# Performance work log

Measured on AMD Instinct MI355X. Metric: run time of the kernel, lower is better.

## Reference

```python
import jax, jax.numpy as jnp
import numpy as np

BRANCH = 16   # children per internal node
DEPTH = 4     # levels 0..4, leaves at level 4
IN = 512
HID = 512

def _level_sizes():
    return [BRANCH ** d for d in range(DEPTH + 1)]

def setup_inputs() -> dict:
    key = jax.random.key(0)
    ks = jax.random.split(key, 9)
    N = sum(_level_sizes())  # 69905
    x = jax.random.normal(ks[0], (N, IN), dtype=jnp.float32)
    s = 1.0 / np.sqrt(IN + HID)  # torch nn.Linear default init bound
    def lin(kw, kb):
        w = jax.random.uniform(kw, (HID, IN + HID), jnp.float32, -s, s)
        b = jax.random.uniform(kb, (HID,), jnp.float32, -s, s)
        return w, b
    wi_w, wi_b = lin(ks[1], ks[2])
    wf_w, wf_b = lin(ks[3], ks[4])
    wo_w, wo_b = lin(ks[5], ks[6])
    wu_w, wu_b = lin(ks[7], ks[8])
    return {"x": x, "wi_w": wi_w, "wi_b": wi_b, "wf_w": wf_w, "wf_b": wf_b,
            "wo_w": wo_w, "wo_b": wo_b, "wu_w": wu_w, "wu_b": wu_b}

def reference(x, wi_w, wi_b, wf_w, wf_b, wo_w, wo_b, wu_w, wu_b):
    sizes = _level_sizes()
    offs = np.concatenate([[0], np.cumsum(sizes)])
    levels = [x[offs[d]:offs[d + 1]] for d in range(DEPTH + 1)]

    def gates(xh):
        i = jax.nn.sigmoid(xh @ wi_w.T + wi_b)
        o = jax.nn.sigmoid(xh @ wo_w.T + wo_b)
        u = jnp.tanh(xh @ wu_w.T + wu_b)
        return i, o, u

    # leaf_forward: h_prev = 0, no forget terms
    Xl = levels[DEPTH]
    xh = jnp.concatenate([Xl, jnp.zeros((Xl.shape[0], HID), Xl.dtype)], axis=1)
    i, o, u = gates(xh)
    C = i * u
    H = o * jnp.tanh(C)

    # node_forward, bottom-up. Faithful quirk of the source: the forget gate
    # is computed on the child CELL state (cat(x, c_k)), not the hidden state.
    for d in range(DEPTH - 1, -1, -1):
        Xd = levels[d]                      # [n, IN]
        n = Xd.shape[0]
        Hc = H.reshape(n, BRANCH, HID)      # children hidden
        Cc = C.reshape(n, BRANCH, HID)      # children cell
        h_sum = Hc.sum(axis=1)
        xh = jnp.concatenate([Xd, h_sum], axis=1)
        i, o, u = gates(xh)
        xc = jnp.concatenate([jnp.broadcast_to(Xd[:, None, :], (n, BRANCH, IN)), Cc], axis=-1)
        f = jax.nn.sigmoid(jnp.einsum('nbk,hk->nbh', xc, wf_w) + wf_b)
        C = i * u + (f * Cc).sum(axis=1)
        H = o * jnp.tanh(C)

    return H[0], C[0]
```

## Files before the change

kernel.cpp:

```cpp
#include <hip/hip_runtime.h>
#include <stdint.h>
#include <stddef.h>


typedef __bf16 bf16x8 __attribute__((ext_vector_type(8)));
typedef float  f32x4  __attribute__((ext_vector_type(4)));
typedef void __attribute__((address_space(3))) lds_void_t;
typedef void __attribute__((address_space(1))) gbl_void_t;

__device__ __forceinline__ uint16_t f2bf(float f) {
  union { __bf16 b; uint16_t u; } v;
  v.b = (__bf16)f;
  return v.u;
}
__device__ __forceinline__ float bf2f(uint16_t u) {
  union { uint32_t u; float f; } v; v.u = (uint32_t)u << 16;
  return v.f;
}
__device__ __forceinline__ float sig_(float x) {
  return __builtin_amdgcn_rcpf(1.0f + __expf(-x));
}
__device__ __forceinline__ float tanh_(float x) {
  return __builtin_fmaf(2.f,
      __builtin_amdgcn_rcpf(1.f + __expf(-2.f * x)), -1.f);
}

__global__ void k_conv_x(const float4* __restrict__ src,
                         ushort4* __restrict__ dst, long n4) {
  long i = blockIdx.x * (long)blockDim.x + threadIdx.x;
  long stride = (long)gridDim.x * blockDim.x;
  for (; i < n4; i += stride) {
    float4 v = src[i];
    ushort4 r;
    r.x = f2bf(v.x); r.y = f2bf(v.y); r.z = f2bf(v.z); r.w = f2bf(v.w);
    dst[i] = r;
  }
}
__global__ void k_conv_w(const float4* __restrict__ w0,
                         const float4* __restrict__ w1,
                         const float4* __restrict__ w2,
                         const float4* __restrict__ w3,
                         ushort4* __restrict__ dst) {
  const long per4 = (long)512 * 1024 / 4;
  long i = blockIdx.x * (long)blockDim.x + threadIdx.x;
  long stride = (long)gridDim.x * blockDim.x;
  for (; i < 4 * per4; i += stride) {
    long seg = i / per4, off2 = i - seg * per4;
    const float4* s = (seg == 0) ? w0 : (seg == 1) ? w1 : (seg == 2) ? w2 : w3;
    float4 v = s[off2];
    ushort4 r;
    r.x = f2bf(v.x); r.y = f2bf(v.y); r.z = f2bf(v.z); r.w = f2bf(v.w);
    dst[i] = r;
  }
}

#define BM 128
#define BN 128
#define BK 32

__global__ __launch_bounds__(256)
void k_gemm_bt(const uint16_t* __restrict__ A, int lda,
               const uint16_t* __restrict__ B, int ldb,
               float* __restrict__ C, int ldc, int K) {
  __shared__ uint16_t As[BM * BK];
  __shared__ uint16_t Bs[BN * BK];
  const int tid = threadIdx.x, lane = tid & 63, wave = tid >> 6;
  const int lrow = lane & 15, quad = lane >> 4;
  const int wm = (wave >> 1) * 64, wn = (wave & 1) * 64;
  const long tm = blockIdx.x, tn = blockIdx.y;
  f32x4 acc[4][4] = {};
  const int srow = lane >> 2, scol = (lane & 3) * 8;
  for (int k0 = 0; k0 < K; k0 += BK) {
#pragma unroll
    for (int i = 0; i < 2; ++i) {
      int row = i * 64 + wave * 16 + srow;
      const uint16_t* gp = A + (tm * BM + row) * (long)lda + k0 + scol;
      __builtin_amdgcn_global_load_lds((gbl_void_t*)(uintptr_t)gp,
          (lds_void_t*)&As[i * 2048 + wave * 512], 16, 0, 0);
    }
#pragma unroll
    for (int i = 0; i < 2; ++i) {
      int row = i * 64 + wave * 16 + srow;
      const uint16_t* gp = B + (tn * BN + row) * (long)ldb + k0 + scol;
      __builtin_amdgcn_global_load_lds((gbl_void_t*)(uintptr_t)gp,
          (lds_void_t*)&Bs[i * 2048 + wave * 512], 16, 0, 0);
    }
    __syncthreads();
    bf16x8 a[4], b[4];
#pragma unroll
    for (int f = 0; f < 4; ++f)
      a[f] = *(const bf16x8*)&As[(wm + f * 16 + lrow) * BK + quad * 8];
#pragma unroll
    for (int f = 0; f < 4; ++f)
      b[f] = *(const bf16x8*)&Bs[(wn + f * 16 + lrow) * BK + quad * 8];
#pragma unroll
    for (int fm = 0; fm < 4; ++fm)
#pragma unroll
      for (int fn = 0; fn < 4; ++fn)
        acc[fm][fn] = __builtin_amdgcn_mfma_f32_16x16x32_bf16(
            a[fm], b[fn], acc[fm][fn], 0, 0, 0);
    __syncthreads();
  }
#pragma unroll
  for (int fm = 0; fm < 4; ++fm)
#pragma unroll
    for (int fn = 0; fn < 4; ++fn) {
      long col  = tn * BN + wn + fn * 16 + lrow;
      long row0 = tm * BM + wm + fm * 16 + quad * 4;
#pragma unroll
      for (int r = 0; r < 4; ++r)
        C[(row0 + r) * (long)ldc + col] = acc[fm][fn][r];
    }
}

template <bool HAS_F>
__global__ __launch_bounds__(256, 3)
void k_level(const uint16_t* __restrict__ A, int lda, int K,
             const uint16_t* __restrict__ Wg,
             const float* __restrict__ bi, const float* __restrict__ bo,
             const float* __restrict__ bu,
             const float* __restrict__ Fpart,
             uint16_t* __restrict__ Cbf,
             const uint16_t* __restrict__ Xnext,
             uint16_t* __restrict__ xh_next) {
  __shared__ uint16_t As[128 * 64];
  __shared__ uint16_t Bs[192 * 64];
  const int tid = threadIdx.x, lane = tid & 63, wave = tid >> 6;
  const int lrow = lane & 15, quad = lane >> 4;
  const int wm = (wave >> 1) * 64, wn = (wave & 1) * 32;

  long tm, tn;
  {
    const int nTm = (int)(gridDim.x >> 3);
    int b = blockIdx.x;
    if ((nTm & 7) == 0) {
      int x = b & 7, j = b >> 3, per = nTm >> 3;
      tn = j & 7; tm = (long)x * per + (j >> 3);
    } else { tm = b >> 3; tn = b & 7; }
  }

  f32x4 acc[3][4][2] = {};

  const int srow = lane >> 3;
  const int scol = (((lane & 7) ^ srow) << 3);
  const int rsw = lrow & 7;
  const int pc[2] = { ((0 + quad) ^ rsw) << 3, ((4 + quad) ^ rsw) << 3 };

  for (int k0 = 0; k0 < K; k0 += 64) {
#pragma unroll
    for (int j = 0; j < 4; ++j) {
      int row = wave * 32 + j * 8 + srow;
      const uint16_t* gp = A + (tm * 128 + row) * (long)lda + k0 + scol;
      __builtin_amdgcn_global_load_lds((gbl_void_t*)(uintptr_t)gp,
          (lds_void_t*)&As[(wave * 32 + j * 8) * 64], 16, 0, 0);
    }
#pragma unroll
    for (int j = 0; j < 6; ++j) {
      int cc = wave * 6 + j;
      int g  = cc >> 3;
      long grow = (long)g * 512 + tn * 64 + (cc & 7) * 8 + srow;
      const uint16_t* gp = Wg + grow * 1024 + k0 + scol;
      __builtin_amdgcn_global_load_lds((gbl_void_t*)(uintptr_t)gp,
          (lds_void_t*)&Bs[cc * 512], 16, 0, 0);
    }
    __syncthreads();

#pragma unroll
    for (int h = 0; h < 2; ++h) {
      bf16x8 a[4];
#pragma unroll
      for (int f = 0; f < 4; ++f)
        a[f] = *(const bf16x8*)&As[(wm + f * 16 + lrow) * 64 + pc[h]];
#pragma unroll
      for (int g = 0; g < 3; ++g) {
        bf16x8 b0 = *(const bf16x8*)&Bs[(g * 64 + wn + lrow) * 64 + pc[h]];
        bf16x8 b1 = *(const bf16x8*)&Bs[(g * 64 + wn + 16 + lrow) * 64 +
                                        pc[h]];
#pragma unroll
        for (int fm = 0; fm < 4; ++fm) {
          acc[g][fm][0] = __builtin_amdgcn_mfma_f32_16x16x32_bf16(
              a[fm], b0, acc[g][fm][0], 0, 0, 0);
          acc[g][fm][1] = __builtin_amdgcn_mfma_f32_16x16x32_bf16(
              a[fm], b1, acc[g][fm][1], 0, 0, 0);
        }
      }
    }
    __syncthreads();
  }

#pragma unroll
  for (int fn = 0; fn < 2; ++fn) {
    long col = tn * 64 + wn + fn * 16 + lrow;
    float biv = bi[col], bov = bo[col], buv = bu[col];
#pragma unroll
    for (int fm = 0; fm < 4; ++fm) {
      long row0 = tm * 128 + wm + fm * 16 + quad * 4;
      long pg   = tm * 8 + (wm >> 4) + fm;
      float hs = 0.f;
#pragma unroll
      for (int r = 0; r < 4; ++r) {
        long row = row0 + r;
        float iv = sig_(acc[0][fm][fn][r] + biv);
        float ov = sig_(acc[1][fm][fn][r] + bov);
        float uv = tanh_(acc[2][fm][fn][r] + buv);
        float c  = iv * uv;
        if (HAS_F) c += Fpart[row * 512 + col];
        Cbf[row * 512 + col] = f2bf(c);
        hs += ov * tanh_(c);
      }
      hs += __shfl_xor(hs, 16, 64);
      hs += __shfl_xor(hs, 32, 64);
      if (quad == 0) {
        xh_next[pg * 1024 + col]       = Xnext[pg * 512 + col];
        xh_next[pg * 1024 + 512 + col] = f2bf(hs);
      }
    }
  }
}

__global__ __launch_bounds__(256, 3)
void k_fc_combine(const uint16_t* __restrict__ Cbf,
                  const uint16_t* __restrict__ Wfc, int ldb,
                  const float* __restrict__ Fx,
                  const float* __restrict__ bfb,
                  float* __restrict__ Fpart) {
  __shared__ uint16_t As[128 * 64];
  __shared__ uint16_t Bs[128 * 64];
  const int tid = threadIdx.x, lane = tid & 63, wave = tid >> 6;
  const int lrow = lane & 15, quad = lane >> 4;
  const int wm = (wave >> 1) * 64, wn = (wave & 1) * 64;
  long tm, tn;
  {
    const int nTm = (int)(gridDim.x >> 2);
    int b = blockIdx.x;
    if ((nTm & 7) == 0) {
      int x = b & 7, j = b >> 3, per = nTm >> 3;
      tn = j & 3; tm = (long)x * per + (j >> 2);
    } else { tm = b >> 2; tn = b & 3; }
  }
  const int lda = 512;
  f32x4 acc[4][4] = {};

  const int srow = lane >> 3;
  const int scol = (((lane & 7) ^ srow) << 3);
  const int rsw = lrow & 7;
  const int pc[2] = { ((0 + quad) ^ rsw) << 3, ((4 + quad) ^ rsw) << 3 };

  for (int k0 = 0; k0 < 512; k0 += 64) {
#pragma unroll
    for (int j = 0; j < 4; ++j) {
      int row = wave * 32 + j * 8 + srow;
      const uint16_t* gp = Cbf + (tm * BM + row) * (long)lda + k0 + scol;
      __builtin_amdgcn_global_load_lds((gbl_void_t*)(uintptr_t)gp,
          (lds_void_t*)&As[(wave * 32 + j * 8) * 64], 16, 0, 0);
    }
#pragma unroll
    for (int j = 0; j < 4; ++j) {
      int row = wave * 32 + j * 8 + srow;
      const uint16_t* gp = Wfc + (tn * BN + row) * (long)ldb + k0 + scol;
      __builtin_amdgcn_global_load_lds((gbl_void_t*)(uintptr_t)gp,
          (lds_void_t*)&Bs[(wave * 32 + j * 8) * 64], 16, 0, 0);
    }
    __syncthreads();
#pragma unroll
    for (int h = 0; h < 2; ++h) {
      bf16x8 a[4], b[4];
#pragma unroll
      for (int f = 0; f < 4; ++f)
        a[f] = *(const bf16x8*)&As[(wm + f * 16 + lrow) * 64 + pc[h]];
#pragma unroll
      for (int f = 0; f < 4; ++f)
        b[f] = *(const bf16x8*)&Bs[(wn + f * 16 + lrow) * 64 + pc[h]];
#pragma unroll
      for (int fm = 0; fm < 4; ++fm)
#pragma unroll
        for (int fn = 0; fn < 4; ++fn)
          acc[fm][fn] = __builtin_amdgcn_mfma_f32_16x16x32_bf16(
              a[fm], b[fn], acc[fm][fn], 0, 0, 0);
    }
    __syncthreads();
  }
#pragma unroll
  for (int fm = 0; fm < 4; ++fm) {
    long pg   = tm * 8 + (wm >> 4) + fm;
    long row0 = tm * BM + wm + fm * 16 + quad * 4;
#pragma unroll
    for (int fn = 0; fn < 4; ++fn) {
      long col = tn * BN + wn + fn * 16 + lrow;
      float fx = Fx[pg * 512 + col] + bfb[col];
      float t = 0.f;
#pragma unroll
      for (int r = 0; r < 4; ++r)
        t += sig_(fx + acc[fm][fn][r]) * bf2f(Cbf[(row0 + r) * 512 + col]);
      t += __shfl_xor(t, 16, 64);
      t += __shfl_xor(t, 32, 64);
      if (quad == 0) Fpart[pg * 512 + col] = t;
    }
  }
}

__global__ void k_dot_bb(const uint16_t* __restrict__ A, int lda,
                         const uint16_t* __restrict__ B, int ldb,
                         float* __restrict__ C, int ldc,
                         int M, int N, int K) {
  int wid  = (int)((blockIdx.x * (long)blockDim.x + threadIdx.x) >> 6);
  int lane = threadIdx.x & 63;
  if (wid >= M * N) return;
  int m = wid / N, n = wid - m * N;
  const uint16_t* a = A + (long)m * lda;
  const uint16_t* b = B + (long)n * ldb;
  int per = K >> 6, k0 = lane * per;
  float s = 0.f;
  for (int j = 0; j < per; j += 4) {
    ushort4 av = *(const ushort4*)(a + k0 + j);
    ushort4 bv = *(const ushort4*)(b + k0 + j);
    s += bf2f(av.x) * bf2f(bv.x) + bf2f(av.y) * bf2f(bv.y)
       + bf2f(av.z) * bf2f(bv.z) + bf2f(av.w) * bf2f(bv.w);
  }
#pragma unroll
  for (int off = 32; off; off >>= 1) s += __shfl_xor(s, off, 64);
  if (lane == 0) C[(long)m * ldc + n] = s;
}
__global__ void k_dot_f32(const float* __restrict__ A, int lda,
                          const float* __restrict__ B, int ldb,
                          float* __restrict__ C, int ldc,
                          int M, int N, int K) {
  int wid  = (int)((blockIdx.x * (long)blockDim.x + threadIdx.x) >> 6);
  int lane = threadIdx.x & 63;
  if (wid >= M * N) return;
  int m = wid / N, n = wid - m * N;
  const float* a = A + (long)m * lda;
  const float* b = B + (long)n * ldb;
  int per = K >> 6, k0 = lane * per;
  float s = 0.f;
  for (int j = 0; j < per; j += 4) {
    float4 av = *(const float4*)(a + k0 + j);
    float4 bv = *(const float4*)(b + k0 + j);
    s += av.x * bv.x + av.y * bv.y + av.z * bv.z + av.w * bv.w;
  }
#pragma unroll
  for (int off = 32; off; off >>= 1) s += __shfl_xor(s, off, 64);
  if (lane == 0) C[(long)m * ldc + n] = s;
}

__global__ void k_hsum_xh4(const float* __restrict__ Hc,
                           const uint16_t* __restrict__ xd,
                           uint16_t* __restrict__ xh, int n) {
  long idx = blockIdx.x * (long)blockDim.x + threadIdx.x;
  if (idx >= (long)n * 128) return;
  long p = idx >> 7; int hq = (int)(idx & 127) << 2;
  const float* hp = Hc + (p << 4) * 512 + hq;
  float4 s = {0.f, 0.f, 0.f, 0.f};
#pragma unroll
  for (int b = 0; b < 16; ++b) {
    float4 v = *(const float4*)(hp + b * 512);
    s.x += v.x; s.y += v.y; s.z += v.z; s.w += v.w;
  }
  *(ushort4*)(xh + p * 1024 + hq) = *(const ushort4*)(xd + p * 512 + hq);
  ushort4 hw = {f2bf(s.x), f2bf(s.y), f2bf(s.z), f2bf(s.w)};
  *(ushort4*)(xh + p * 1024 + 512 + hq) = hw;
}

__global__ void k_combine4(const float* __restrict__ Fc,
                           const float* __restrict__ Fx,
                           const float* __restrict__ bfb,
                           const float* __restrict__ Cc,
                           float* __restrict__ Fpart, int nParents) {
  long idx = blockIdx.x * (long)blockDim.x + threadIdx.x;
  if (idx >= (long)nParents * 128) return;
  long pl = idx >> 7; int hq = (int)(idx & 127) << 2;
  float4 fxv = *(const float4*)(Fx + pl * 512 + hq);
  float4 bfv = *(const float4*)(bfb + hq);
  float fx0 = fxv.x + bfv.x, fx1 = fxv.y + bfv.y;
  float fx2 = fxv.z + bfv.z, fx3 = fxv.w + bfv.w;
  float a0 = 0.f, a1 = 0.f, a2 = 0.f, a3 = 0.f;
#pragma unroll 4
  for (int b = 0; b < 16; ++b) {
    long cl = pl * 16 + b;
    float4 f = *(const float4*)(Fc + cl * 512 + hq);
    float4 c = *(const float4*)(Cc + cl * 512 + hq);
    a0 += sig_(fx0 + f.x) * c.x;
    a1 += sig_(fx1 + f.y) * c.y;
    a2 += sig_(fx2 + f.z) * c.z;
    a3 += sig_(fx3 + f.w) * c.w;
  }
  float4 r = {a0, a1, a2, a3};
  *(float4*)(Fpart + pl * 512 + hq) = r;
}

__global__ void k_final4(const float* __restrict__ G,
                         const float* __restrict__ Fpart,
                         const float* __restrict__ bi,
                         const float* __restrict__ bo,
                         const float* __restrict__ bu,
                         float* __restrict__ H, float* __restrict__ Cv,
                         uint16_t* __restrict__ Cbf, int n) {
  long idx = blockIdx.x * (long)blockDim.x + threadIdx.x;
  if (idx >= (long)n * 128) return;
  long p = idx >> 7; int hq = (int)(idx & 127) << 2;
  const float* g = G + p * 1536;
  float4 gi = *(const float4*)(g + hq);
  float4 go = *(const float4*)(g + 512 + hq);
  float4 gu = *(const float4*)(g + 1024 + hq);
  float4 b_i = *(const float4*)(bi + hq);
  float4 b_o = *(const float4*)(bo + hq);
  float4 b_u = *(const float4*)(bu + hq);
  float4 fp = *(const float4*)(Fpart + p * 512 + hq);
  const float* gip = &gi.x; const float* gop = &go.x; const float* gup = &gu.x;
  const float* bip = &b_i.x; const float* bop = &b_o.x; const float* bup = &b_u.x;
  const float* fpp = &fp.x;
  float4 hv, cv;
  float* hvp = &hv.x; float* cvp = &cv.x;
  ushort4 cw; unsigned short* cwp = &cw.x;
#pragma unroll
  for (int j = 0; j < 4; ++j) {
    float iv = sig_(gip[j] + bip[j]);
    float ov = sig_(gop[j] + bop[j]);
    float uv = tanh_(gup[j] + bup[j]);
    float c  = iv * uv + fpp[j];
    cvp[j] = c;
    cwp[j] = f2bf(c);
    hvp[j] = ov * tanh_(c);
  }
  *(float4*)(H  + p * 512 + hq) = hv;
  *(float4*)(Cv + p * 512 + hq) = cv;
  *(ushort4*)(Cbf + p * 512 + hq) = cw;
}

extern "C" void kernel_launch(void* const* d_in, const int* in_sizes, int n_in,
                              void* d_out, int out_size, void* d_ws, size_t ws_size,
                              hipStream_t stream) {
  const float* x    = (const float*)d_in[0];
  const float* wi_w = (const float*)d_in[1];
  const float* wi_b = (const float*)d_in[2];
  const float* wf_w = (const float*)d_in[3];
  const float* wf_b = (const float*)d_in[4];
  const float* wo_w = (const float*)d_in[5];
  const float* wo_b = (const float*)d_in[6];
  const float* wu_w = (const float*)d_in[7];
  const float* wu_b = (const float*)d_in[8];
  (void)in_sizes; (void)n_in; (void)out_size; (void)ws_size;

  static const long offs[5] = {0, 1, 17, 273, 4369};
  const long NTOT = 69905;

  char* ws = (char*)d_ws;
  size_t off = 0;
  auto alloc = [&](size_t bytes) -> void* {
    void* p = ws + off;
    off += (bytes + 255) & ~(size_t)255;
    return p;
  };
  uint16_t* Xbf   = (uint16_t*)alloc(NTOT * 512 * 2);
  uint16_t* Wgw   = (uint16_t*)alloc((size_t)2048 * 1024 * 2);
  uint16_t* Wg    = Wgw;
  uint16_t* Wf    = Wgw + (size_t)1536 * 1024;
  float*    FxAll = (float*)alloc((size_t)4480 * 512 * 4);
  uint16_t* Cbf   = (uint16_t*)alloc((size_t)65536 * 512 * 2);
  uint16_t* CbfU  = (uint16_t*)alloc((size_t)4096 * 512 * 2);
  uint16_t* CbfU2 = (uint16_t*)alloc((size_t)256 * 512 * 2);
  uint16_t* xhA   = (uint16_t*)alloc((size_t)4096 * 1024 * 2);
  uint16_t* xhB   = (uint16_t*)alloc((size_t)256 * 1024 * 2);
  uint16_t* xhC   = (uint16_t*)alloc((size_t)16 * 1024 * 2);
  float*    Fpart = (float*)alloc((size_t)4096 * 512 * 4);
  float*    Gf    = (float*)alloc((size_t)16 * 1536 * 4);
  float*    Fc    = (float*)alloc((size_t)16 * 512 * 4);
  float*    HupA  = (float*)alloc((size_t)16 * 512 * 4);
  float*    CupA  = (float*)alloc((size_t)16 * 512 * 4);

  auto blks = [](long n) { return (int)((n + 255) / 256); };

  {
    long n4 = NTOT * 512 / 4;
    k_conv_x<<<8192, 256, 0, stream>>>((const float4*)x, (ushort4*)Xbf, n4);
    k_conv_w<<<2048, 256, 0, stream>>>((const float4*)wi_w, (const float4*)wo_w,
                                       (const float4*)wu_w, (const float4*)wf_w,
                                       (ushort4*)Wgw);
  }

  {
    dim3 grid(35, 4);
    k_gemm_bt<<<grid, 256, 0, stream>>>(Xbf, 512, Wf, 1024, FxAll, 512, 512);
  }

  k_level<false><<<4096, 256, 0, stream>>>(
      Xbf + offs[4] * 512, 512, 512, Wg, wi_b, wo_b, wu_b, nullptr,
      Cbf, Xbf + offs[3] * 512, xhA);
  k_fc_combine<<<2048, 256, 0, stream>>>(Cbf, Wf + 512, 1024,
                                         FxAll + offs[3] * 512, wf_b, Fpart);

  k_level<true><<<256, 256, 0, stream>>>(
      xhA, 1024, 1024, Wg, wi_b, wo_b, wu_b, Fpart,
      CbfU, Xbf + offs[2] * 512, xhB);
  k_fc_combine<<<128, 256, 0, stream>>>(CbfU, Wf + 512, 1024,
                                        FxAll + offs[2] * 512, wf_b, Fpart);

  k_level<true><<<16, 256, 0, stream>>>(
      xhB, 1024, 1024, Wg, wi_b, wo_b, wu_b, Fpart,
      CbfU2, Xbf + offs[1] * 512, xhC);
  k_fc_combine<<<8, 256, 0, stream>>>(CbfU2, Wf + 512, 1024,
                                      FxAll + offs[1] * 512, wf_b, Fpart);

  {
    long waves = 16L * 1536;
    k_dot_bb<<<(int)((waves * 64 + 255) / 256), 256, 0, stream>>>(
        xhC, 1024, Wg, 1024, Gf, 1536, 16, 1536, 1024);
    k_final4<<<blks(16L * 128), 256, 0, stream>>>(
        Gf, Fpart, wi_b, wo_b, wu_b, HupA, CupA, CbfU2, 16);
  }

  k_hsum_xh4<<<1, 256, 0, stream>>>(HupA, Xbf + offs[0] * 512, xhC, 1);
  {
    long waves = 1536;
    k_dot_bb<<<(int)((waves * 64 + 255) / 256), 256, 0, stream>>>(
        xhC, 1024, Wg, 1024, Gf, 1536, 1, 1536, 1024);
  }
  {
    long waves = 16L * 512;
    k_dot_f32<<<(int)((waves * 64 + 255) / 256), 256, 0, stream>>>(
        CupA, 512, wf_w + 512, 1024, Fc, 512, 16, 512, 512);
  }
  k_combine4<<<1, 256, 0, stream>>>(Fc, FxAll, wf_b, CupA, Fpart, 1);
  k_final4<<<1, 256, 0, stream>>>(
      Gf, Fpart, wi_b, wo_b, wu_b,
      (float*)d_out, (float*)d_out + 512, CbfU2, 1);
}
```

Measured before the change: 523.8 us.

## Double-buffer LDS with async prefetch and 512-thread 256-row tiles in level GEMMs

Changes k_level and k_fc_combine to use 8 waves per block with 256-row M tiles. Both kernels now double-buffer the LDS stages, prefetching two K-tiles ahead with global_load_lds, and use vmcnt waits, raw barriers and setprio to overlap loads with MFMA work. The goal is to hide global-memory latency and halve per-block weight reloads. In exchange, LDS use roughly doubles, occupancy drops, and the small upper-level launches get even fewer blocks.

Result: slower. 572.1 us (+9.2%).

```diff
diff --git a/kernel.cpp b/kernel.cpp
--- a/kernel.cpp
+++ b/kernel.cpp
@@ -7,6 +7,8 @@
 typedef float  f32x4  __attribute__((ext_vector_type(4)));
 typedef void __attribute__((address_space(3))) lds_void_t;
 typedef void __attribute__((address_space(1))) gbl_void_t;
+
+#define WAITVM(n) asm volatile("s_waitcnt vmcnt(" #n ")" ::: "memory")
 
 __device__ __forceinline__ uint16_t f2bf(float f) {
   union { __bf16 b; uint16_t u; } v;
@@ -114,7 +116,7 @@
 }
 
 template <bool HAS_F>
-__global__ __launch_bounds__(256, 3)
+__global__ __launch_bounds__(512, 2)
 void k_level(const uint16_t* __restrict__ A, int lda, int K,
              const uint16_t* __restrict__ Wg,
              const float* __restrict__ bi, const float* __restrict__ bo,
@@ -123,8 +125,8 @@
              uint16_t* __restrict__ Cbf,
              const uint16_t* __restrict__ Xnext,
              uint16_t* __restrict__ xh_next) {
-  __shared__ uint16_t As[128 * 64];
-  __shared__ uint16_t Bs[192 * 64];
+  __shared__ uint16_t As[2][256 * 64];
+  __shared__ uint16_t Bs[2][192 * 64];
   const int tid = threadIdx.x, lane = tid & 63, wave = tid >> 6;
   const int lrow = lane & 15, quad = lane >> 4;
   const int wm = (wave >> 1) * 64, wn = (wave & 1) * 32;
@@ -146,36 +148,40 @@
   const int rsw = lrow & 7;
   const int pc[2] = { ((0 + quad) ^ rsw) << 3, ((4 + quad) ^ rsw) << 3 };
 
-  for (int k0 = 0; k0 < K; k0 += 64) {
+  auto stage = [&](int kt, int buf) {
+    int k0 = kt * 64;
 #pragma unroll
     for (int j = 0; j < 4; ++j) {
-      int row = wave * 32 + j * 8 + srow;
-      const uint16_t* gp = A + (tm * 128 + row) * (long)lda + k0 + scol;
+      int grp = wave * 4 + j;
+      const uint16_t* gp = A + (tm * 256 + grp * 8 + srow) * (long)lda +
+                           k0 + scol;
       __builtin_amdgcn_global_load_lds((gbl_void_t*)(uintptr_t)gp,
-          (lds_void_t*)&As[(wave * 32 + j * 8) * 64], 16, 0, 0);
-    }
-#pragma unroll
-    for (int j = 0; j < 6; ++j) {
-      int cc = wave * 6 + j;
+          (lds_void_t*)&As[buf][grp * 512], 16, 0, 0);
+    }
+#pragma unroll
+    for (int j = 0; j < 3; ++j) {
+      int cc = wave * 3 + j;
       int g  = cc >> 3;
       long grow = (long)g * 512 + tn * 64 + (cc & 7) * 8 + srow;
       const uint16_t* gp = Wg + grow * 1024 + k0 + scol;
       __builtin_amdgcn_global_load_lds((gbl_void_t*)(uintptr_t)gp,
-          (lds_void_t*)&Bs[cc * 512], 16, 0, 0);
-    }
-    __syncthreads();
-
+          (lds_void_t*)&Bs[buf][cc * 512], 16, 0, 0);
+    }
+  };
+
+  auto compute = [&](int buf) {
 #pragma unroll
     for (int h = 0; h < 2; ++h) {
       bf16x8 a[4];
 #pragma unroll
       for (int f = 0; f < 4; ++f)
-        a[f] = *(const bf16x8*)&As[(wm + f * 16 + lrow) * 64 + pc[h]];
+        a[f] = *(const bf16x8*)&As[buf][(wm + f * 16 + lrow) * 64 + pc[h]];
 #pragma unroll
       for (int g = 0; g < 3; ++g) {
-        bf16x8 b0 = *(const bf16x8*)&Bs[(g * 64 + wn + lrow) * 64 + pc[h]];
-        bf16x8 b1 = *(const bf16x8*)&Bs[(g * 64 + wn + 16 + lrow) * 64 +
-                                        pc[h]];
+        bf16x8 b0 = *(const bf16x8*)&Bs[buf][(g * 64 + wn + lrow) * 64 +
+                                            pc[h]];
+        bf16x8 b1 = *(const bf16x8*)&Bs[buf][(g * 64 + wn + 16 + lrow) * 64 +
+                                            pc[h]];
 #pragma unroll
         for (int fm = 0; fm < 4; ++fm) {
           acc[g][fm][0] = __builtin_amdgcn_mfma_f32_16x16x32_bf16(
@@ -185,7 +191,19 @@
         }
       }
     }
-    __syncthreads();
+  };
+
+  const int NT = K >> 6;
+  stage(0, 0);
+  stage(1, 1);
+  for (int t = 0; t < NT; ++t) {
+    WAITVM(7);
+    __builtin_amdgcn_s_barrier();
+    __builtin_amdgcn_s_setprio(1);
+    compute(t & 1);
+    __builtin_amdgcn_s_setprio(0);
+    __builtin_amdgcn_s_barrier();
+    if (t + 2 < NT) stage(t + 2, t & 1);
   }
 
 #pragma unroll
@@ -194,8 +212,8 @@
     float biv = bi[col], bov = bo[col], buv = bu[col];
 #pragma unroll
     for (int fm = 0; fm < 4; ++fm) {
-      long row0 = tm * 128 + wm + fm * 16 + quad * 4;
-      long pg   = tm * 8 + (wm >> 4) + fm;
+      long row0 = tm * 256 + wm + fm * 16 + quad * 4;
+      long pg   = tm * 16 + (wm >> 4) + fm;
       float hs = 0.f;
 #pragma unroll
       for (int r = 0; r < 4; ++r) {
@@ -218,14 +236,14 @@
   }
 }
 
-__global__ __launch_bounds__(256, 3)
+__global__ __launch_bounds__(512, 2)
 void k_fc_combine(const uint16_t* __restrict__ Cbf,
                   const uint16_t* __restrict__ Wfc, int ldb,
                   const float* __restrict__ Fx,
                   const float* __restrict__ bfb,
                   float* __restrict__ Fpart) {
-  __shared__ uint16_t As[128 * 64];
-  __shared__ uint16_t Bs[128 * 64];
+  __shared__ uint16_t As[2][256 * 64];
+  __shared__ uint16_t Bs[2][128 * 64];
   const int tid = threadIdx.x, lane = tid & 63, wave = tid >> 6;
   const int lrow = lane & 15, quad = lane >> 4;
   const int wm = (wave >> 1) * 64, wn = (wave & 1) * 64;
@@ -246,31 +264,36 @@
   const int rsw = lrow & 7;
   const int pc[2] = { ((0 + quad) ^ rsw) << 3, ((4 + quad) ^ rsw) << 3 };
 
-  for (int k0 = 0; k0 < 512; k0 += 64) {
+  auto stage = [&](int kt, int buf) {
+    int k0 = kt * 64;
 #pragma unroll
     for (int j = 0; j < 4; ++j) {
-      int row = wave * 32 + j * 8 + srow;
-      const uint16_t* gp = Cbf + (tm * BM + row) * (long)lda + k0 + scol;
+      int grp = wave * 4 + j;
+      const uint16_t* gp = Cbf + (tm * 256 + grp * 8 + srow) * (long)lda +
+                           k0 + scol;
       __builtin_amdgcn_global_load_lds((gbl_void_t*)(uintptr_t)gp,
-          (lds_void_t*)&As[(wave * 32 + j * 8) * 64], 16, 0, 0);
-    }
-#pragma unroll
-    for (int j = 0; j < 4; ++j) {
-      int row = wave * 32 + j * 8 + srow;
-      const uint16_t* gp = Wfc + (tn * BN + row) * (long)ldb + k0 + scol;
+          (lds_void_t*)&As[buf][grp * 512], 16, 0, 0);
+    }
+#pragma unroll
+    for (int j = 0; j < 2; ++j) {
+      int cc = wave * 2 + j;
+      const uint16_t* gp = Wfc + (tn * 128 + cc * 8 + srow) * (long)ldb +
+                           k0 + scol;
       __builtin_amdgcn_global_load_lds((gbl_void_t*)(uintptr_t)gp,
-          (lds_void_t*)&Bs[(wave * 32 + j * 8) * 64], 16, 0, 0);
-    }
-    __syncthreads();
+          (lds_void_t*)&Bs[buf][cc * 512], 16, 0, 0);
+    }
+  };
+
+  auto compute = [&](int buf) {
 #pragma unroll
     for (int h = 0; h < 2; ++h) {
       bf16x8 a[4], b[4];
 #pragma unroll
       for (int f = 0; f < 4; ++f)
-        a[f] = *(const bf16x8*)&As[(wm + f * 16 + lrow) * 64 + pc[h]];
+        a[f] = *(const bf16x8*)&As[buf][(wm + f * 16 + lrow) * 64 + pc[h]];
 #pragma unroll
       for (int f = 0; f < 4; ++f)
-        b[f] = *(const bf16x8*)&Bs[(wn + f * 16 + lrow) * 64 + pc[h]];
+        b[f] = *(const bf16x8*)&Bs[buf][(wn + f * 16 + lrow) * 64 + pc[h]];
 #pragma unroll
       for (int fm = 0; fm < 4; ++fm)
 #pragma unroll
@@ -278,15 +301,28 @@
           acc[fm][fn] = __builtin_amdgcn_mfma_f32_16x16x32_bf16(
               a[fm], b[fn], acc[fm][fn], 0, 0, 0);
     }
-    __syncthreads();
-  }
+  };
+
+  const int NT = 8;
+  stage(0, 0);
+  stage(1, 1);
+  for (int t = 0; t < NT; ++t) {
+    WAITVM(6);
+    __builtin_amdgcn_s_barrier();
+    __builtin_amdgcn_s_setprio(1);
+    compute(t & 1);
+    __builtin_amdgcn_s_setprio(0);
+    __builtin_amdgcn_s_barrier();
+    if (t + 2 < NT) stage(t + 2, t & 1);
+  }
+
 #pragma unroll
   for (int fm = 0; fm < 4; ++fm) {
-    long pg   = tm * 8 + (wm >> 4) + fm;
-    long row0 = tm * BM + wm + fm * 16 + quad * 4;
+    long pg   = tm * 16 + (wm >> 4) + fm;
+    long row0 = tm * 256 + wm + fm * 16 + quad * 4;
 #pragma unroll
     for (int fn = 0; fn < 4; ++fn) {
-      long col = tn * BN + wn + fn * 16 + lrow;
+      long col = tn * 128 + wn + fn * 16 + lrow;
       float fx = Fx[pg * 512 + col] + bfb[col];
       float t = 0.f;
 #pragma unroll
@@ -483,22 +519,22 @@
     k_gemm_bt<<<grid, 256, 0, stream>>>(Xbf, 512, Wf, 1024, FxAll, 512, 512);
   }
 
-  k_level<false><<<4096, 256, 0, stream>>>(
+  k_level<false><<<2048, 512, 0, stream>>>(
       Xbf + offs[4] * 512, 512, 512, Wg, wi_b, wo_b, wu_b, nullptr,
       Cbf, Xbf + offs[3] * 512, xhA);
-  k_fc_combine<<<2048, 256, 0, stream>>>(Cbf, Wf + 512, 1024,
+  k_fc_combine<<<1024, 512, 0, stream>>>(Cbf, Wf + 512, 1024,
                                          FxAll + offs[3] * 512, wf_b, Fpart);
 
-  k_level<true><<<256, 256, 0, stream>>>(
+  k_level<true><<<128, 512, 0, stream>>>(
       xhA, 1024, 1024, Wg, wi_b, wo_b, wu_b, Fpart,
       CbfU, Xbf + offs[2] * 512, xhB);
-  k_fc_combine<<<128, 256, 0, stream>>>(CbfU, Wf + 512, 1024,
-                                        FxAll + offs[2] * 512, wf_b, Fpart);
-
-  k_level<true><<<16, 256, 0, stream>>>(
+  k_fc_combine<<<64, 512, 0, stream>>>(CbfU, Wf + 512, 1024,
+                                       FxAll + offs[2] * 512, wf_b, Fpart);
+
+  k_level<true><<<8, 512, 0, stream>>>(
       xhB, 1024, 1024, Wg, wi_b, wo_b, wu_b, Fpart,
       CbfU2, Xbf + offs[1] * 512, xhC);
-  k_fc_combine<<<8, 256, 0, stream>>>(CbfU2, Wf + 512, 1024,
+  k_fc_combine<<<4, 512, 0, stream>>>(CbfU2, Wf + 512, 1024,
                                       FxAll + offs[1] * 512, wf_b, Fpart);
 
   {
```
